# Kernel tuning notes

Hardware: AMD Instinct MI355X
Metric: run time of the kernel (lower is better)

Reference implementation:

```python
import jax, jax.numpy as jnp
import numpy as np

N_HIDDEN_LAYERS = 9  # 32->32 middle layers (plus input 1->32 and output 32->1)
HID = 32
SLOPE = 0.01  # LeakyReLU negative_slope


def leaky_relu(x):
    return jnp.where(x >= 0, x, SLOPE * x)


def setup_inputs() -> dict:
    key = jax.random.key(0)
    ks = jax.random.split(key, 8)
    N = 1048576
    x = jax.random.normal(ks[0], (N,), dtype=jnp.float32)
    # PyTorch Linear init: U(-1/sqrt(fan_in), 1/sqrt(fan_in))
    def u(k, shape, fan_in):
        b = 1.0 / np.sqrt(fan_in)
        return jax.random.uniform(k, shape, jnp.float32, -b, b)
    W_in = u(ks[1], (1, HID), 1)
    b_in = u(ks[2], (HID,), 1)
    W_hid = u(ks[3], (N_HIDDEN_LAYERS, HID, HID), HID)
    b_hid = u(ks[4], (N_HIDDEN_LAYERS, HID), HID)
    W_out = u(ks[5], (HID, 1), HID)
    b_out = u(ks[6], (1,), HID)
    return {"x": x, "W_in": W_in, "b_in": b_in, "W_hid": W_hid,
            "b_hid": b_hid, "W_out": W_out, "b_out": b_out}


def reference(x, W_in, b_in, W_hid, b_hid, W_out, b_out):
    N = x.shape[0]
    h = x[:, None]  # [N, 1], mirrors x.reshape(N, 1)
    h = leaky_relu(h @ W_in + b_in)  # [N, 32]
    def step(h, wb):
        W, b = wb
        return leaky_relu(h @ W + b), None
    h, _ = jax.lax.scan(step, h, (W_hid, b_hid))
    out = h @ W_out + b_out  # [N, 1]
    return out.reshape(1, N)
```

## Files before the change

### kernel.cpp

```cpp
#include <hip/hip_runtime.h>

#define NLAYERS 9
#define HID 32
#define SLOPE 0.01f

typedef _Float16 v2h __attribute__((ext_vector_type(2)));
typedef _Float16 v8h __attribute__((ext_vector_type(8)));
typedef float v4f __attribute__((ext_vector_type(4)));

#define NCHAIN 6

union U8 { v8h v; v2h p[4]; };

__device__ __forceinline__ v2h pk_cvt(float a, float b) {
    return __builtin_bit_cast(v2h, __builtin_amdgcn_cvt_pkrtz(a, b));
}
__device__ __forceinline__ v2h leaky2(v2h t, v2h s) {
    return __builtin_elementwise_max(t, t * s);
}
__device__ __forceinline__ int umap(int g, int j) {
    return 4 * g + (j & 3) + 16 * (j >> 2);
}

__global__ __launch_bounds__(256, 2) void mlp_mfma_kernel(
    const float* __restrict__ x,
    const float* __restrict__ W_in,
    const float* __restrict__ b_in,
    const float* __restrict__ W_hid,
    const float* __restrict__ b_hid,
    const float* __restrict__ W_out,
    const float* __restrict__ b_out,
    float* __restrict__ out, int N)
{
    __shared__ __align__(16) _Float16 wA_sh[NLAYERS][2][64][8];
    __shared__ __align__(64) float bc_sh[NLAYERS][2][16];

    const int tid = threadIdx.x;
    for (int t = tid; t < NLAYERS * 2 * 64; t += blockDim.x) {
        int l = t >> 7, r = t & 127, tt = (r >> 6) & 1, ln = r & 63;
        int i = ln & 15, gg = ln >> 4;
        const float* Wl = W_hid + l * HID * HID;
        v8h w;
#pragma unroll
        for (int j = 0; j < 8; ++j)
            w[j] = (_Float16)Wl[umap(gg, j) * HID + 16 * tt + i];
        *(v8h*)&wA_sh[l][tt][ln][0] = w;
    }
    for (int t = tid; t < NLAYERS * HID; t += blockDim.x)
        ((float*)bc_sh)[t] = b_hid[t];
    __syncthreads();

    const int lane = tid & 63;
    const int g    = lane >> 4;
    const int col  = lane & 15;

    v2h win2[4], bin2[4], wout2[4];
#pragma unroll
    for (int jj = 0; jj < 4; ++jj) {
        int u0 = umap(g, 2 * jj), u1 = umap(g, 2 * jj + 1);
        win2[jj]  = v2h{(_Float16)W_in[u0],  (_Float16)W_in[u1]};
        bin2[jj]  = v2h{(_Float16)b_in[u0],  (_Float16)b_in[u1]};
        wout2[jj] = v2h{(_Float16)W_out[u0], (_Float16)W_out[u1]};
    }
    const float bo = b_out[0];
    const v2h slope2 = v2h{(_Float16)SLOPE, (_Float16)SLOPE};

    const int nwaves = (gridDim.x * blockDim.x) >> 6;
    const int wid    = (blockIdx.x * blockDim.x + tid) >> 6;
    const int niter  = (N + NCHAIN * 32 - 1) / (NCHAIN * 32);

    v2h xc2[NCHAIN];
#pragma unroll
    for (int c = 0; c < NCHAIN; ++c) xc2[c] = v2h{(_Float16)0.f, (_Float16)0.f};
    if (wid < niter) {
#pragma unroll
        for (int c = 0; c < NCHAIN; ++c) {
            int i0 = wid * (NCHAIN * 32) + c * 32 + col;
            int i1 = i0 + 16;
            float a = (i0 < N) ? x[i0] : 0.0f;
            float b = (i1 < N) ? x[i1] : 0.0f;
            xc2[c] = pk_cvt(a, b);
        }
    }

    for (int it = wid; it < niter; it += nwaves) {
        v2h xn2[NCHAIN];
#pragma unroll
        for (int c = 0; c < NCHAIN; ++c) xn2[c] = v2h{(_Float16)0.f, (_Float16)0.f};
        {
            int nit = it + nwaves;
            if (nit < niter) {
#pragma unroll
                for (int c = 0; c < NCHAIN; ++c) {
                    int i0 = nit * (NCHAIN * 32) + c * 32 + col;
                    int i1 = i0 + 16;
                    float a = (i0 < N) ? x[i0] : 0.0f;
                    float b = (i1 < N) ? x[i1] : 0.0f;
                    xn2[c] = pk_cvt(a, b);
                }
            }
        }

        U8 f[NCHAIN][2];
#pragma unroll
        for (int c = 0; c < NCHAIN; ++c)
#pragma unroll
            for (int nh = 0; nh < 2; ++nh) {
                _Float16 xh = xc2[c][nh];
                v2h x2 = v2h{xh, xh};
#pragma unroll
                for (int jj = 0; jj < 4; ++jj)
                    f[c][nh].p[jj] = leaky2(x2 * win2[jj] + bin2[jj], slope2);
            }

        v8h wA0 = *(const v8h*)&wA_sh[0][0][lane][0];
        v8h wA1 = *(const v8h*)&wA_sh[0][1][lane][0];
        v4f bc0 = *(const v4f*)&bc_sh[0][0][4 * g];
        v4f bc1 = *(const v4f*)&bc_sh[0][1][4 * g];
#pragma unroll 1
        for (int l = 0; l < NLAYERS; ++l) {
            const int lnx = (l + 1 < NLAYERS) ? l + 1 : l;
            v8h wA0n = *(const v8h*)&wA_sh[lnx][0][lane][0];
            v8h wA1n = *(const v8h*)&wA_sh[lnx][1][lane][0];
            v4f bc0n = *(const v4f*)&bc_sh[lnx][0][4 * g];
            v4f bc1n = *(const v4f*)&bc_sh[lnx][1][4 * g];

            v4f A0[2][4], A1[2][4], A2[2][4];
#pragma unroll
            for (int q = 0; q < 2; ++q) {
                A0[q][0] = __builtin_amdgcn_mfma_f32_16x16x32_f16(wA0, f[q][0].v, bc0, 0, 0, 0);
                A0[q][1] = __builtin_amdgcn_mfma_f32_16x16x32_f16(wA0, f[q][1].v, bc0, 0, 0, 0);
                A0[q][2] = __builtin_amdgcn_mfma_f32_16x16x32_f16(wA1, f[q][0].v, bc1, 0, 0, 0);
                A0[q][3] = __builtin_amdgcn_mfma_f32_16x16x32_f16(wA1, f[q][1].v, bc1, 0, 0, 0);
            }
#pragma unroll
            for (int q = 0; q < 2; ++q) {
                A1[q][0] = __builtin_amdgcn_mfma_f32_16x16x32_f16(wA0, f[2 + q][0].v, bc0, 0, 0, 0);
                A1[q][1] = __builtin_amdgcn_mfma_f32_16x16x32_f16(wA0, f[2 + q][1].v, bc0, 0, 0, 0);
                A1[q][2] = __builtin_amdgcn_mfma_f32_16x16x32_f16(wA1, f[2 + q][0].v, bc1, 0, 0, 0);
                A1[q][3] = __builtin_amdgcn_mfma_f32_16x16x32_f16(wA1, f[2 + q][1].v, bc1, 0, 0, 0);
            }
#pragma unroll
            for (int q = 0; q < 2; ++q) {
                f[q][0].p[0] = leaky2(pk_cvt(A0[q][0][0], A0[q][0][1]), slope2);
                f[q][0].p[1] = leaky2(pk_cvt(A0[q][0][2], A0[q][0][3]), slope2);
                f[q][0].p[2] = leaky2(pk_cvt(A0[q][2][0], A0[q][2][1]), slope2);
                f[q][0].p[3] = leaky2(pk_cvt(A0[q][2][2], A0[q][2][3]), slope2);
                f[q][1].p[0] = leaky2(pk_cvt(A0[q][1][0], A0[q][1][1]), slope2);
                f[q][1].p[1] = leaky2(pk_cvt(A0[q][1][2], A0[q][1][3]), slope2);
                f[q][1].p[2] = leaky2(pk_cvt(A0[q][3][0], A0[q][3][1]), slope2);
                f[q][1].p[3] = leaky2(pk_cvt(A0[q][3][2], A0[q][3][3]), slope2);
            }
#pragma unroll
            for (int q = 0; q < 2; ++q) {
                A2[q][0] = __builtin_amdgcn_mfma_f32_16x16x32_f16(wA0, f[4 + q][0].v, bc0, 0, 0, 0);
                A2[q][1] = __builtin_amdgcn_mfma_f32_16x16x32_f16(wA0, f[4 + q][1].v, bc0, 0, 0, 0);
                A2[q][2] = __builtin_amdgcn_mfma_f32_16x16x32_f16(wA1, f[4 + q][0].v, bc1, 0, 0, 0);
                A2[q][3] = __builtin_amdgcn_mfma_f32_16x16x32_f16(wA1, f[4 + q][1].v, bc1, 0, 0, 0);
            }
#pragma unroll
            for (int q = 0; q < 2; ++q) {
                f[2 + q][0].p[0] = leaky2(pk_cvt(A1[q][0][0], A1[q][0][1]), slope2);
                f[2 + q][0].p[1] = leaky2(pk_cvt(A1[q][0][2], A1[q][0][3]), slope2);
                f[2 + q][0].p[2] = leaky2(pk_cvt(A1[q][2][0], A1[q][2][1]), slope2);
                f[2 + q][0].p[3] = leaky2(pk_cvt(A1[q][2][2], A1[q][2][3]), slope2);
                f[2 + q][1].p[0] = leaky2(pk_cvt(A1[q][1][0], A1[q][1][1]), slope2);
                f[2 + q][1].p[1] = leaky2(pk_cvt(A1[q][1][2], A1[q][1][3]), slope2);
                f[2 + q][1].p[2] = leaky2(pk_cvt(A1[q][3][0], A1[q][3][1]), slope2);
                f[2 + q][1].p[3] = leaky2(pk_cvt(A1[q][3][2], A1[q][3][3]), slope2);
            }
#pragma unroll
            for (int q = 0; q < 2; ++q) {
                f[4 + q][0].p[0] = leaky2(pk_cvt(A2[q][0][0], A2[q][0][1]), slope2);
                f[4 + q][0].p[1] = leaky2(pk_cvt(A2[q][0][2], A2[q][0][3]), slope2);
                f[4 + q][0].p[2] = leaky2(pk_cvt(A2[q][2][0], A2[q][2][1]), slope2);
                f[4 + q][0].p[3] = leaky2(pk_cvt(A2[q][2][2], A2[q][2][3]), slope2);
                f[4 + q][1].p[0] = leaky2(pk_cvt(A2[q][1][0], A2[q][1][1]), slope2);
                f[4 + q][1].p[1] = leaky2(pk_cvt(A2[q][1][2], A2[q][1][3]), slope2);
                f[4 + q][1].p[2] = leaky2(pk_cvt(A2[q][3][0], A2[q][3][1]), slope2);
                f[4 + q][1].p[3] = leaky2(pk_cvt(A2[q][3][2], A2[q][3][3]), slope2);
            }

            wA0 = wA0n; wA1 = wA1n; bc0 = bc0n; bc1 = bc1n;
        }

#pragma unroll
        for (int c = 0; c < NCHAIN; ++c)
#pragma unroll
            for (int nh = 0; nh < 2; ++nh) {
                float p = 0.0f;
#pragma unroll
                for (int jj = 0; jj < 4; ++jj)
                    p = __builtin_amdgcn_fdot2(f[c][nh].p[jj], wout2[jj], p, false);
                p += __shfl_xor(p, 16, 64);
                p += __shfl_xor(p, 32, 64);
                float o = p + bo;
                int idx = it * (NCHAIN * 32) + c * 32 + 16 * nh + col;
                if (((2 * c + nh) & 3) == g && idx < N) out[idx] = o;
            }

#pragma unroll
        for (int c = 0; c < NCHAIN; ++c) xc2[c] = xn2[c];
    }
}

extern "C" void kernel_launch(void* const* d_in, const int* in_sizes, int n_in,
                              void* d_out, int out_size, void* d_ws, size_t ws_size,
                              hipStream_t stream) {
    const float* x     = (const float*)d_in[0];
    const float* W_in  = (const float*)d_in[1];
    const float* b_in  = (const float*)d_in[2];
    const float* W_hid = (const float*)d_in[3];
    const float* b_hid = (const float*)d_in[4];
    const float* W_out = (const float*)d_in[5];
    const float* b_out = (const float*)d_in[6];
    float* out = (float*)d_out;

    int N = in_sizes[0];
    dim3 block(256);
    dim3 grid(512);
    mlp_mfma_kernel<<<grid, block, 0, stream>>>(x, W_in, b_in, W_hid, b_hid,
                                                W_out, b_out, out, N);
}
```

Measured before the change: 97.21 us.

## Trade per-wave MFMA chains for higher occupancy and a larger grid

Cuts independent MFMA chains per wave from six to two, raises launch_bounds minimum blocks per CU from 2 to 4, and enlarges the grid from 512 to 1280 blocks. The per-layer weight prefetch (double buffering) is dropped, and weights are loaded directly each layer. The intent is to hide MFMA latency through more resident waves instead of instruction-level parallelism within a wave. The risk is that each wave stalls more on MFMA dependencies and the per-layer LDS loads without the prefetch, and that scheduling overhead grows.

```diff
diff --git a/kernel.cpp b/kernel.cpp
--- a/kernel.cpp
+++ b/kernel.cpp
@@ -8,7 +8,7 @@
 typedef _Float16 v8h __attribute__((ext_vector_type(8)));
 typedef float v4f __attribute__((ext_vector_type(4)));
 
-#define NCHAIN 6
+#define NCHAIN 2
 
 union U8 { v8h v; v2h p[4]; };
 
@@ -22,7 +22,7 @@
     return 4 * g + (j & 3) + 16 * (j >> 2);
 }
 
-__global__ __launch_bounds__(256, 2) void mlp_mfma_kernel(
+__global__ __launch_bounds__(256, 4) void mlp_mfma_kernel(
     const float* __restrict__ x,
     const float* __restrict__ W_in,
     const float* __restrict__ b_in,
@@ -113,75 +113,39 @@
                     f[c][nh].p[jj] = leaky2(x2 * win2[jj] + bin2[jj], slope2);
             }
 
-        v8h wA0 = *(const v8h*)&wA_sh[0][0][lane][0];
-        v8h wA1 = *(const v8h*)&wA_sh[0][1][lane][0];
-        v4f bc0 = *(const v4f*)&bc_sh[0][0][4 * g];
-        v4f bc1 = *(const v4f*)&bc_sh[0][1][4 * g];
 #pragma unroll 1
         for (int l = 0; l < NLAYERS; ++l) {
-            const int lnx = (l + 1 < NLAYERS) ? l + 1 : l;
-            v8h wA0n = *(const v8h*)&wA_sh[lnx][0][lane][0];
-            v8h wA1n = *(const v8h*)&wA_sh[lnx][1][lane][0];
-            v4f bc0n = *(const v4f*)&bc_sh[lnx][0][4 * g];
-            v4f bc1n = *(const v4f*)&bc_sh[lnx][1][4 * g];
+            v8h wA0 = *(const v8h*)&wA_sh[l][0][lane][0];
+            v8h wA1 = *(const v8h*)&wA_sh[l][1][lane][0];
+            v4f bc0 = *(const v4f*)&bc_sh[l][0][4 * g];
+            v4f bc1 = *(const v4f*)&bc_sh[l][1][4 * g];
 
-            v4f A0[2][4], A1[2][4], A2[2][4];
-#pragma unroll
-            for (int q = 0; q < 2; ++q) {
-                A0[q][0] = __builtin_amdgcn_mfma_f32_16x16x32_f16(wA0, f[q][0].v, bc0, 0, 0, 0);
-                A0[q][1] = __builtin_amdgcn_mfma_f32_16x16x32_f16(wA0, f[q][1].v, bc0, 0, 0, 0);
-                A0[q][2] = __builtin_amdgcn_mfma_f32_16x16x32_f16(wA1, f[q][0].v, bc1, 0, 0, 0);
-                A0[q][3] = __builtin_amdgcn_mfma_f32_16x16x32_f16(wA1, f[q][1].v, bc1, 0, 0, 0);
-            }
-#pragma unroll
-            for (int q = 0; q < 2; ++q) {
-                A1[q][0] = __builtin_amdgcn_mfma_f32_16x16x32_f16(wA0, f[2 + q][0].v, bc0, 0, 0, 0);
-                A1[q][1] = __builtin_amdgcn_mfma_f32_16x16x32_f16(wA0, f[2 + q][1].v, bc0, 0, 0, 0);
-                A1[q][2] = __builtin_amdgcn_mfma_f32_16x16x32_f16(wA1, f[2 + q][0].v, bc1, 0, 0, 0);
-                A1[q][3] = __builtin_amdgcn_mfma_f32_16x16x32_f16(wA1, f[2 + q][1].v, bc1, 0, 0, 0);
-            }
-#pragma unroll
-            for (int q = 0; q < 2; ++q) {
-                f[q][0].p[0] = leaky2(pk_cvt(A0[q][0][0], A0[q][0][1]), slope2);
-                f[q][0].p[1] = leaky2(pk_cvt(A0[q][0][2], A0[q][0][3]), slope2);
-                f[q][0].p[2] = leaky2(pk_cvt(A0[q][2][0], A0[q][2][1]), slope2);
-                f[q][0].p[3] = leaky2(pk_cvt(A0[q][2][2], A0[q][2][3]), slope2);
-                f[q][1].p[0] = leaky2(pk_cvt(A0[q][1][0], A0[q][1][1]), slope2);
-                f[q][1].p[1] = leaky2(pk_cvt(A0[q][1][2], A0[q][1][3]), slope2);
-                f[q][1].p[2] = leaky2(pk_cvt(A0[q][3][0], A0[q][3][1]), slope2);
-                f[q][1].p[3] = leaky2(pk_cvt(A0[q][3][2], A0[q][3][3]), slope2);
-            }
-#pragma unroll
-            for (int q = 0; q < 2; ++q) {
-                A2[q][0] = __builtin_amdgcn_mfma_f32_16x16x32_f16(wA0, f[4 + q][0].v, bc0, 0, 0, 0);
-                A2[q][1] = __builtin_amdgcn_mfma_f32_16x16x32_f16(wA0, f[4 + q][1].v, bc0, 0, 0, 0);
-                A2[q][2] = __builtin_amdgcn_mfma_f32_16x16x32_f16(wA1, f[4 + q][0].v, bc1, 0, 0, 0);
-                A2[q][3] = __builtin_amdgcn_mfma_f32_16x16x32_f16(wA1, f[4 + q][1].v, bc1, 0, 0, 0);
-            }
-#pragma unroll
-            for (int q = 0; q < 2; ++q) {
-                f[2 + q][0].p[0] = leaky2(pk_cvt(A1[q][0][0], A1[q][0][1]), slope2);
-                f[2 + q][0].p[1] = leaky2(pk_cvt(A1[q][0][2], A1[q][0][3]), slope2);
-                f[2 + q][0].p[2] = leaky2(pk_cvt(A1[q][2][0], A1[q][2][1]), slope2);
-                f[2 + q][0].p[3] = leaky2(pk_cvt(A1[q][2][2], A1[q][2][3]), slope2);
-                f[2 + q][1].p[0] = leaky2(pk_cvt(A1[q][1][0], A1[q][1][1]), slope2);
-                f[2 + q][1].p[1] = leaky2(pk_cvt(A1[q][1][2], A1[q][1][3]), slope2);
-                f[2 + q][1].p[2] = leaky2(pk_cvt(A1[q][3][0], A1[q][3][1]), slope2);
-                f[2 + q][1].p[3] = leaky2(pk_cvt(A1[q][3][2], A1[q][3][3]), slope2);
-            }
-#pragma unroll
-            for (int q = 0; q < 2; ++q) {
-                f[4 + q][0].p[0] = leaky2(pk_cvt(A2[q][0][0], A2[q][0][1]), slope2);
-                f[4 + q][0].p[1] = leaky2(pk_cvt(A2[q][0][2], A2[q][0][3]), slope2);
-                f[4 + q][0].p[2] = leaky2(pk_cvt(A2[q][2][0], A2[q][2][1]), slope2);
-                f[4 + q][0].p[3] = leaky2(pk_cvt(A2[q][2][2], A2[q][2][3]), slope2);
-                f[4 + q][1].p[0] = leaky2(pk_cvt(A2[q][1][0], A2[q][1][1]), slope2);
-                f[4 + q][1].p[1] = leaky2(pk_cvt(A2[q][1][2], A2[q][1][3]), slope2);
-                f[4 + q][1].p[2] = leaky2(pk_cvt(A2[q][3][0], A2[q][3][1]), slope2);
-                f[4 + q][1].p[3] = leaky2(pk_cvt(A2[q][3][2], A2[q][3][3]), slope2);
-            }
+            v4f A0[4], A1[4];
+            A0[0] = __builtin_amdgcn_mfma_f32_16x16x32_f16(wA0, f[0][0].v, bc0, 0, 0, 0);
+            A0[1] = __builtin_amdgcn_mfma_f32_16x16x32_f16(wA0, f[0][1].v, bc0, 0, 0, 0);
+            A0[2] = __builtin_amdgcn_mfma_f32_16x16x32_f16(wA1, f[0][0].v, bc1, 0, 0, 0);
+            A0[3] = __builtin_amdgcn_mfma_f32_16x16x32_f16(wA1, f[0][1].v, bc1, 0, 0, 0);
+            A1[0] = __builtin_amdgcn_mfma_f32_16x16x32_f16(wA0, f[1][0].v, bc0, 0, 0, 0);
+            A1[1] = __builtin_amdgcn_mfma_f32_16x16x32_f16(wA0, f[1][1].v, bc0, 0, 0, 0);
+            A1[2] = __builtin_amdgcn_mfma_f32_16x16x32_f16(wA1, f[1][0].v, bc1, 0, 0, 0);
+            A1[3] = __builtin_amdgcn_mfma_f32_16x16x32_f16(wA1, f[1][1].v, bc1, 0, 0, 0);
 
-            wA0 = wA0n; wA1 = wA1n; bc0 = bc0n; bc1 = bc1n;
+            f[0][0].p[0] = leaky2(pk_cvt(A0[0][0], A0[0][1]), slope2);
+            f[0][0].p[1] = leaky2(pk_cvt(A0[0][2], A0[0][3]), slope2);
+            f[0][0].p[2] = leaky2(pk_cvt(A0[2][0], A0[2][1]), slope2);
+            f[0][0].p[3] = leaky2(pk_cvt(A0[2][2], A0[2][3]), slope2);
+            f[0][1].p[0] = leaky2(pk_cvt(A0[1][0], A0[1][1]), slope2);
+            f[0][1].p[1] = leaky2(pk_cvt(A0[1][2], A0[1][3]), slope2);
+            f[0][1].p[2] = leaky2(pk_cvt(A0[3][0], A0[3][1]), slope2);
+            f[0][1].p[3] = leaky2(pk_cvt(A0[3][2], A0[3][3]), slope2);
+            f[1][0].p[0] = leaky2(pk_cvt(A1[0][0], A1[0][1]), slope2);
+            f[1][0].p[1] = leaky2(pk_cvt(A1[0][2], A1[0][3]), slope2);
+            f[1][0].p[2] = leaky2(pk_cvt(A1[2][0], A1[2][1]), slope2);
+            f[1][0].p[3] = leaky2(pk_cvt(A1[2][2], A1[2][3]), slope2);
+            f[1][1].p[0] = leaky2(pk_cvt(A1[1][0], A1[1][1]), slope2);
+            f[1][1].p[1] = leaky2(pk_cvt(A1[1][2], A1[1][3]), slope2);
+            f[1][1].p[2] = leaky2(pk_cvt(A1[3][0], A1[3][1]), slope2);
+            f[1][1].p[3] = leaky2(pk_cvt(A1[3][2], A1[3][3]), slope2);
         }
 
 #pragma unroll
@@ -196,7 +160,7 @@
                 p += __shfl_xor(p, 32, 64);
                 float o = p + bo;
                 int idx = it * (NCHAIN * 32) + c * 32 + 16 * nh + col;
-                if (((2 * c + nh) & 3) == g && idx < N) out[idx] = o;
+                if (g == 2 * c + nh && idx < N) out[idx] = o;
             }
 
 #pragma unroll
@@ -218,7 +182,7 @@
 
     int N = in_sizes[0];
     dim3 block(256);
-    dim3 grid(512);
+    dim3 grid(1280);
     mlp_mfma_kernel<<<grid, block, 0, stream>>>(x, W_in, b_in, W_hid, b_hid,
                                                 W_out, b_out, out, N);
 }
```

Result: faster. 93.33 us (-4.0%).
